# Optimization experiments

Hardware: AMD Instinct MI355X
Metric: run time of the kernel (lower is better)

Reference implementation:

```python
import jax, jax.numpy as jnp
import numpy as np

B, D, T, STRIDE = 16, 512, 2048, 4
SIGMA_SQUARE = 5.0
L = -(-T // STRIDE)  # ceil(T/stride) = 512


def setup_inputs() -> dict:
    key = jax.random.key(0)
    k1, k2, k3 = jax.random.split(key, 3)
    x = jax.random.normal(k1, (B, D, T), dtype=jnp.float32)
    # score conv: Conv1d(hdim, 1, 1, bias=False) == a single weight vector over D
    # (zero-initialized in the module; use small random values for a meaningful test)
    w = jax.random.normal(k2, (D,), dtype=jnp.float32) * 0.01
    x_lengths = jax.random.randint(k3, (B,), T // 2, T + 1)
    x_mask = jnp.arange(T)[None, :] < x_lengths[:, None]  # [B, T] bool
    return {"x": x, "w": w, "x_mask": x_mask, "x_lengths": x_lengths}


def reference(x, w, x_mask, x_lengths):
    maskf = x_mask.astype(x.dtype)  # [B, T]
    z_lengths = jnp.ceil(x_lengths.astype(x.dtype) / STRIDE).astype(jnp.int32)  # [B]
    z_mask = x_mask[:, ::STRIDE]  # [B, L]

    # score = exp(conv1x1(x)) * mask ; cum-sum position score
    score = jnp.exp(jnp.einsum('bdt,d->bt', x, w)) * maskf  # [B, T]
    cum = jnp.cumsum(score, axis=-1)  # [B, T]
    norm = (cum - cum[:, :1]) / (cum[:, -1:] - cum[:, :1]) \
           * (z_lengths[:, None].astype(x.dtype) - 1.0)  # [B, T]

    # monotonic-rate regularizer (get_score_loss)
    diff = norm[:, 1:] - norm[:, :-1]  # [B, T-1]
    score_loss = ((jax.nn.relu(diff - 1.0) * maskf[:, 1:]).sum(axis=-1)
                  / (x_lengths.astype(x.dtype) - 1.0)).mean()

    # masked Gaussian distance -> softmax over T -> alignment-weighted sum
    idx = jnp.arange(L, dtype=x.dtype)  # [L]
    dist = -SIGMA_SQUARE * (idx[None, None, :] - norm[:, :, None]) ** 2  # [B, T, L]
    dist = jnp.swapaxes(dist, 1, 2)  # [B, L, T]
    dist = jnp.where(x_mask[:, None, :], dist, -jnp.inf)
    alignment = jax.nn.softmax(dist, axis=-1) * z_mask[:, :, None].astype(x.dtype)  # [B, L, T]

    z = jnp.einsum('blt,bdt->bdl', alignment, x)  # [B, D, L]
    return z, z_mask, z_lengths, alignment, score_loss
```

## Files before the change

### kernel.cpp

```cpp
#include <hip/hip_runtime.h>
#include <cstddef>

#define Bn 16
#define Dn 512
#define Tn 2048
#define Ln 512
#define NLT 64

typedef float nfloat4 __attribute__((ext_vector_type(4)));

__global__ __launch_bounds__(256) void scorefill_kernel(const float* __restrict__ x,
                                                        const float* __restrict__ w,
                                                        const int* __restrict__ xlen,
                                                        float* __restrict__ score,
                                                        float* __restrict__ align) {
    int bid = blockIdx.x;
    int tid = threadIdx.x;

    if (bid >= 1024) {
        const size_t NT = (size_t)Bn * Ln * Tn / 4;
        nfloat4* a4 = (nfloat4*)align;
        size_t i = (size_t)(bid - 1024) * 256 + tid;
        nfloat4 z4 = {0.f, 0.f, 0.f, 0.f};
        __builtin_nontemporal_store(z4, &a4[i]);
        __builtin_nontemporal_store(z4, &a4[i + NT / 4]);
        __builtin_nontemporal_store(z4, &a4[i + 2 * (NT / 4)]);
        __builtin_nontemporal_store(z4, &a4[i + 3 * (NT / 4)]);
        return;
    }

    int b   = bid >> 6;
    int tc  = bid & 63;
    int xl  = xlen[b];
    int t0c = tc * 32;
    if (t0c >= xl) {
        if (tid < 8)
            *(float4*)&score[b * Tn + t0c + tid * 4] = make_float4(0.f, 0.f, 0.f, 0.f);
        return;
    }
    int tq = tid & 7;
    int dg = tid >> 3;
    int t0 = t0c + tq * 4;
    const float* xb = x + (size_t)b * Dn * Tn + t0;
    float4 acc = make_float4(0.f, 0.f, 0.f, 0.f);
    int dbase = dg * 16;
#pragma unroll
    for (int i = 0; i < 16; ++i) {
        int d = dbase + i;
        float4 v = *(const float4*)&xb[(size_t)d * Tn];
        float wd = w[d];
        acc.x = fmaf(v.x, wd, acc.x);
        acc.y = fmaf(v.y, wd, acc.y);
        acc.z = fmaf(v.z, wd, acc.z);
        acc.w = fmaf(v.w, wd, acc.w);
    }
    __shared__ float4 red[32][8];
    __shared__ float4 red2[8][8];
    red[dg][tq] = acc;
    __syncthreads();
    if (tid < 64) {
        int q = tid & 7, g = tid >> 3;
        float4 s0 = red[g * 4 + 0][q], s1 = red[g * 4 + 1][q];
        float4 s2 = red[g * 4 + 2][q], s3 = red[g * 4 + 3][q];
        float4 s;
        s.x = (s0.x + s1.x) + (s2.x + s3.x);
        s.y = (s0.y + s1.y) + (s2.y + s3.y);
        s.z = (s0.z + s1.z) + (s2.z + s3.z);
        s.w = (s0.w + s1.w) + (s2.w + s3.w);
        red2[g][q] = s;
    }
    __syncthreads();
    if (tid < 8) {
        float4 s = red2[0][tid];
#pragma unroll
        for (int g = 1; g < 8; ++g) {
            float4 r = red2[g][tid];
            s.x += r.x; s.y += r.y; s.z += r.z; s.w += r.w;
        }
        int t = t0c + tid * 4;
        float4 o;
        o.x = (t + 0 < xl) ? __expf(s.x) : 0.f;
        o.y = (t + 1 < xl) ? __expf(s.y) : 0.f;
        o.z = (t + 2 < xl) ? __expf(s.z) : 0.f;
        o.w = (t + 3 < xl) ? __expf(s.w) : 0.f;
        *(float4*)&score[b * Tn + t] = o;
    }
}

__global__ __launch_bounds__(256) void scan_kernel(const float* __restrict__ score,
                                                   const int* __restrict__ xlen,
                                                   float* __restrict__ norm,
                                                   float* __restrict__ loss_part,
                                                   float* __restrict__ zmask_out,
                                                   float* __restrict__ zlen_out,
                                                   int* __restrict__ wlo,
                                                   int* __restrict__ whi,
                                                   float* __restrict__ sMout,
                                                   float* __restrict__ sIout) {
    int b = blockIdx.x, tid = threadIdx.x;
    int xl = xlen[b];
    int zl = (xl + 3) >> 2;
    const float* sc = score + b * Tn;

    __shared__ float sNorm[Tn];
    __shared__ int   sTC[Ln];

    float v[8]; float s = 0.f;
#pragma unroll
    for (int k = 0; k < 8; ++k) { v[k] = sc[tid * 8 + k]; s += v[k]; }

    float ps = s;
#pragma unroll
    for (int off = 1; off < 64; off <<= 1) {
        float n = __shfl_up(ps, off, 64);
        if ((tid & 63) >= off) ps += n;
    }
    __shared__ float wsum[4];
    if ((tid & 63) == 63) wsum[tid >> 6] = ps;
    __syncthreads();
    float base = 0.f;
#pragma unroll
    for (int wv = 0; wv < 4; ++wv) if (wv < (tid >> 6)) base += wsum[wv];
    float total = wsum[0] + wsum[1] + wsum[2] + wsum[3];
    float cum0  = sc[0];
    float scale = (float)(zl - 1) / (total - cum0);

    float run = base + ps - s;
    float nv[8];
#pragma unroll
    for (int k = 0; k < 8; ++k) {
        run += v[k];
        float xx = (run - cum0) * scale;
        nv[k] = xx;
        norm[b * Tn + tid * 8 + k] = xx;
        sNorm[tid * 8 + k] = xx;
    }

    float ls = 0.f;
#pragma unroll
    for (int k = 0; k < 8; ++k) {
        int t = tid * 8 + k;
        if (t >= 1 && t < xl) {
            float diff = v[k] * scale;
            ls += fmaxf(diff - 1.0f, 0.f);
        }
    }
#pragma unroll
    for (int off = 32; off; off >>= 1) ls += __shfl_down(ls, off, 64);
    __shared__ float lw[4];
    if ((tid & 63) == 0) lw[tid >> 6] = ls;

    for (int l = tid; l < Ln; l += 256)
        zmask_out[b * Ln + l] = (l * 4 < xl) ? 1.f : 0.f;
    if (tid == 0) zlen_out[b] = (float)zl;

    for (int i = tid; i < NLT; i += 256) {
        wlo[b * NLT + i] = xl;
        whi[b * NLT + i] = xl;
    }
    for (int l = tid; l < Ln; l += 256) sTC[l] = xl - 1;
    __syncthreads();
    if (tid == 0) loss_part[b] = (lw[0] + lw[1] + lw[2] + lw[3]) / (float)(xl - 1);

#pragma unroll
    for (int k = 0; k < 8; ++k) {
        int t = tid * 8 + k;
        float vv = nv[k];
        float p  = (t == 0) ? -1e9f : sNorm[t - 1];
        int lsr = (int)floorf((p + 1.5f) * 0.125f) + 1; if (lsr < 0) lsr = 0;
        int ler = (int)floorf((vv + 1.5f) * 0.125f);    if (ler > NLT - 1) ler = NLT - 1;
        for (int lt = lsr; lt <= ler; ++lt) wlo[b * NLT + lt] = t;
        int hs = (int)ceilf((p - 8.5f) * 0.125f);       if (hs < 0) hs = 0;
        int he = (int)ceilf((vv - 8.5f) * 0.125f) - 1;  if (he > NLT - 1) he = NLT - 1;
        for (int lt = hs; lt <= he; ++lt) whi[b * NLT + lt] = t;
        int cs = (int)floorf(p) + 1;  if (cs < 0) cs = 0;
        int ce = (int)floorf(vv);     if (ce > Ln - 1) ce = Ln - 1;
        for (int l = cs; l <= ce; ++l) sTC[l] = t;
    }
    __syncthreads();

    for (int l = tid; l < Ln; l += 256) {
        float mv = 0.f, iv = 0.f;
        if (l < zl) {
            int tc2 = sTC[l];
            float d1 = (float)l - sNorm[tc2];
            float m  = -5.f * d1 * d1;
            if (tc2 > 0) { float d0v = (float)l - sNorm[tc2 - 1]; float c = -5.f * d0v * d0v; m = fmaxf(m, c); }
            int lo = (l >= 2) ? sTC[l - 2] : 0;
            int hi = (l + 2 <= zl - 1) ? sTC[l + 2] : xl;
            int tcm1 = (tc2 > 0) ? tc2 - 1 : 0;
            if (lo > tcm1) lo = tcm1;
            int tcp1 = (tc2 + 1 < xl) ? tc2 + 1 : xl;
            if (hi < tcp1) hi = tcp1;
            float ssum = 0.f;
            for (int t = lo; t < hi; ++t) {
                float df = (float)l - sNorm[t];
                ssum += __expf(-5.f * df * df - m);
            }
            mv = m; iv = 1.f / ssum;
        }
        sMout[b * Ln + l] = mv;
        sIout[b * Ln + l] = iv;
    }
}

__global__ __launch_bounds__(256) void z_kernel(const float* __restrict__ x,
                                                const float* __restrict__ norm,
                                                const int* __restrict__ xlen,
                                                const int* __restrict__ wlo,
                                                const int* __restrict__ whi,
                                                const float* __restrict__ sM,
                                                const float* __restrict__ sI,
                                                const float* __restrict__ loss_part,
                                                float* __restrict__ align,
                                                float* __restrict__ z,
                                                float* __restrict__ out_loss) {
    int tid = threadIdx.x;
    int bid = blockIdx.x;
    if (bid == 0 && tid == 0) {
        float s = 0.f;
        for (int i = 0; i < Bn; ++i) s += loss_part[i];
        out_loss[0] = s / (float)Bn;
    }
    int swz = (bid & 7) * 256 + (bid >> 3);
    int b   = swz >> 7;
    int rem = swz & 127;
    int lt  = rem >> 1;
    int dh  = rem & 1;
    int l0  = lt * 8;
    int xl  = xlen[b];
    int zl  = (xl + 3) >> 2;
    int d   = dh * 256 + tid;
    size_t zr = (size_t)(b * Dn + d) * Ln + l0;

    if (l0 >= zl) {
        float4 z4 = make_float4(0.f, 0.f, 0.f, 0.f);
        *(float4*)&z[zr] = z4; *(float4*)&z[zr + 4] = z4;
        return;
    }

    int tlo = wlo[b * NLT + lt];
    int thi = whi[b * NLT + lt];
    if (thi > xl) thi = xl;
    int tA = tlo & ~15;

    __shared__ float sA[64][8];
    const float* nb = norm + b * Tn;
    const float* xr = x + (size_t)(b * Dn + d) * Tn;

    int al = tid >> 5;
    int as = tid & 31;
    float ml = sM[b * Ln + l0 + al];
    float il = sI[b * Ln + l0 + al];
    float lr = (float)(l0 + al);
    float* ar = align + (size_t)(b * Ln + l0 + al) * Tn;

    float acc[8] = {};
    float4 rx[16];

    for (int t0 = tA; t0 < thi; t0 += 64) {
#pragma unroll
        for (int j = 0; j < 16; ++j) {
            int tj = t0 + 4 * j;
            if (tj > Tn - 4) tj = Tn - 4;
            rx[j] = *(const float4*)&xr[tj];
        }
        {
            int t1 = t0 + as, t2 = t1 + 32;
            float a1 = 0.f, a2 = 0.f;
            if (t1 < thi) { float df = lr - nb[t1]; a1 = __expf(fmaf(-5.f * df, df, -ml)) * il; }
            if (t2 < thi) { float df = lr - nb[t2]; a2 = __expf(fmaf(-5.f * df, df, -ml)) * il; }
            sA[as][al] = a1;
            sA[as + 32][al] = a2;
            if (dh == 0) {
                if (t1 < thi) ar[t1] = a1;
                if (t2 < thi) ar[t2] = a2;
            }
        }
        __syncthreads();
#pragma unroll
        for (int c = 0; c < 16; ++c) {
            float4 xv = rx[c];
#pragma unroll
            for (int e = 0; e < 4; ++e) {
                int s = 4 * c + e;
                float xs = ((const float*)&xv)[e];
                float4 a0 = *(const float4*)&sA[s][0];
                float4 a1 = *(const float4*)&sA[s][4];
                acc[0] = fmaf(xs, a0.x, acc[0]);
                acc[1] = fmaf(xs, a0.y, acc[1]);
                acc[2] = fmaf(xs, a0.z, acc[2]);
                acc[3] = fmaf(xs, a0.w, acc[3]);
                acc[4] = fmaf(xs, a1.x, acc[4]);
                acc[5] = fmaf(xs, a1.y, acc[5]);
                acc[6] = fmaf(xs, a1.z, acc[6]);
                acc[7] = fmaf(xs, a1.w, acc[7]);
            }
        }
        __syncthreads();
    }

    *(float4*)&z[zr]     = make_float4(acc[0], acc[1], acc[2], acc[3]);
    *(float4*)&z[zr + 4] = make_float4(acc[4], acc[5], acc[6], acc[7]);
}

extern "C" void kernel_launch(void* const* d_in, const int* in_sizes, int n_in,
                              void* d_out, int out_size, void* d_ws, size_t ws_size,
                              hipStream_t stream) {
    const float* x    = (const float*)d_in[0];
    const float* w    = (const float*)d_in[1];
    const int*   xlen = (const int*)d_in[3];
    float* out = (float*)d_out;

    const size_t OFF_Z     = 0;
    const size_t OFF_ZMASK = (size_t)Bn * Dn * Ln;
    const size_t OFF_ZLEN  = OFF_ZMASK + (size_t)Bn * Ln;
    const size_t OFF_ALIGN = OFF_ZLEN + Bn;
    const size_t OFF_LOSS  = OFF_ALIGN + (size_t)Bn * Ln * Tn;

    float* score     = (float*)d_ws;
    float* norm      = score + (size_t)Bn * Tn;
    float* loss_part = norm + (size_t)Bn * Tn;
    int*   wlo       = (int*)(loss_part + Bn);
    int*   whi       = wlo + Bn * NLT;
    float* sMw       = (float*)(whi + Bn * NLT);
    float* sIw       = sMw + (size_t)Bn * Ln;

    scorefill_kernel<<<1024 + 4096, 256, 0, stream>>>(x, w, xlen, score,
                                                      out + OFF_ALIGN);
    scan_kernel<<<Bn, 256, 0, stream>>>(score, xlen, norm, loss_part,
                                        out + OFF_ZMASK, out + OFF_ZLEN,
                                        wlo, whi, sMw, sIw);
    z_kernel<<<Bn * NLT * 2, 256, 0, stream>>>(x, norm, xlen, wlo, whi,
                                               sMw, sIw, loss_part,
                                               out + OFF_ALIGN, out + OFF_Z,
                                               out + OFF_LOSS);
}
```

Before: 56.23 us.

## Zero only inactive alignment rows up front and fill out-of-window zeros in z kernel

Previously every element of the 64 MB alignment tensor was zeroed with nontemporal stores, even though the z kernel later overwrote the active band. Now the prefill blocks zero only rows whose l index is at or beyond z_length, and the z kernel zeroes the parts of each active row that lie outside its computed window, splitting that work between the two d-halves. This is meant to remove the redundant double write of the active region. The score kernel also issues all 16 x loads before the FMAs to improve memory-level parallelism. The risk is uneven work across blocks and correctness at the window edges, where the unaligned tail is handled with scalar stores.

```diff
diff --git a/kernel.cpp b/kernel.cpp
--- a/kernel.cpp
+++ b/kernel.cpp
@@ -6,8 +6,6 @@
 #define Tn 2048
 #define Ln 512
 #define NLT 64
-
-typedef float nfloat4 __attribute__((ext_vector_type(4)));
 
 __global__ __launch_bounds__(256) void scorefill_kernel(const float* __restrict__ x,
                                                         const float* __restrict__ w,
@@ -18,14 +16,18 @@
     int tid = threadIdx.x;
 
     if (bid >= 1024) {
-        const size_t NT = (size_t)Bn * Ln * Tn / 4;
-        nfloat4* a4 = (nfloat4*)align;
-        size_t i = (size_t)(bid - 1024) * 256 + tid;
-        nfloat4 z4 = {0.f, 0.f, 0.f, 0.f};
-        __builtin_nontemporal_store(z4, &a4[i]);
-        __builtin_nontemporal_store(z4, &a4[i + NT / 4]);
-        __builtin_nontemporal_store(z4, &a4[i + 2 * (NT / 4)]);
-        __builtin_nontemporal_store(z4, &a4[i + 3 * (NT / 4)]);
+        int r0 = (bid - 1024) * 2;
+        float4 z4 = make_float4(0.f, 0.f, 0.f, 0.f);
+#pragma unroll
+        for (int rr = 0; rr < 2; ++rr) {
+            int r = r0 + rr;
+            int b = r >> 9, l = r & 511;
+            int zl = (xlen[b] + 3) >> 2;
+            if (l < zl) continue;
+            float4* row4 = (float4*)(align + (size_t)r * Tn);
+            row4[tid]       = z4;
+            row4[tid + 256] = z4;
+        }
         return;
     }
 
@@ -41,19 +43,24 @@
     int tq = tid & 7;
     int dg = tid >> 3;
     int t0 = t0c + tq * 4;
-    const float* xb = x + (size_t)b * Dn * Tn + t0;
+    const float* xb = x + (size_t)b * Dn * Tn + (size_t)(dg * 16) * Tn + t0;
+    const float* wb = w + dg * 16;
+
+    float4 rx[16];
+#pragma unroll
+    for (int i = 0; i < 16; ++i)
+        rx[i] = *(const float4*)&xb[(size_t)i * Tn];
+
     float4 acc = make_float4(0.f, 0.f, 0.f, 0.f);
-    int dbase = dg * 16;
 #pragma unroll
     for (int i = 0; i < 16; ++i) {
-        int d = dbase + i;
-        float4 v = *(const float4*)&xb[(size_t)d * Tn];
-        float wd = w[d];
-        acc.x = fmaf(v.x, wd, acc.x);
-        acc.y = fmaf(v.y, wd, acc.y);
-        acc.z = fmaf(v.z, wd, acc.z);
-        acc.w = fmaf(v.w, wd, acc.w);
-    }
+        float wd = wb[i];
+        acc.x = fmaf(rx[i].x, wd, acc.x);
+        acc.y = fmaf(rx[i].y, wd, acc.y);
+        acc.z = fmaf(rx[i].z, wd, acc.z);
+        acc.w = fmaf(rx[i].w, wd, acc.w);
+    }
+
     __shared__ float4 red[32][8];
     __shared__ float4 red2[8][8];
     red[dg][tq] = acc;
@@ -244,6 +251,27 @@
     if (thi > xl) thi = xl;
     int tA = tlo & ~15;
 
+    {
+        int start4 = (thi + 3) & ~3;
+        if (start4 > Tn) start4 = Tn;
+        int rest   = Tn - start4 - tA;
+        if (rest < 0) rest = 0;
+        int mid4   = start4 + ((rest >> 3) << 2);
+        int row    = tid >> 5, lane32 = tid & 31;
+        float* arw = align + (size_t)(b * Ln + l0 + row) * Tn;
+        float4 z4f = make_float4(0.f, 0.f, 0.f, 0.f);
+        if (dh == 0) {
+            for (int q = lane32; q < (tA >> 2); q += 32)
+                ((float4*)arw)[q] = z4f;
+            if (thi + lane32 < start4) arw[thi + lane32] = 0.f;
+            for (int q = (start4 >> 2) + lane32; q < (mid4 >> 2); q += 32)
+                ((float4*)arw)[q] = z4f;
+        } else {
+            for (int q = (mid4 >> 2) + lane32; q < (Tn >> 2); q += 32)
+                ((float4*)arw)[q] = z4f;
+        }
+    }
+
     __shared__ float sA[64][8];
     const float* nb = norm + b * Tn;
     const float* xr = x + (size_t)(b * Dn + d) * Tn;
```

Result: faster. 52.81 us (-6.1%).
